# Optimization experiments

Hardware: AMD Instinct MI355X
Metric: run time of the kernel (lower is better)

Reference implementation:

```python
import jax, jax.numpy as jnp
import numpy as np

B, N, D, H, L = 2, 1024, 256, 4, 6
DH = D // H          # head dim 64
RDIM = DH // 2       # AxialRotaryEmbedding dim = 32 -> output feature size DH
THETA = 0.01


def setup_inputs() -> dict:
    key = jax.random.key(0)
    ks = iter(jax.random.split(key, 80))
    def nrm(shape, s=1.0):
        return jax.random.normal(next(ks), shape, jnp.float32) * s
    size = jnp.array([1024.0, 768.0], jnp.float32)
    inp = {
        'kpts0': jax.random.uniform(next(ks), (B, N, 2), jnp.float32) * size,
        'kpts1': jax.random.uniform(next(ks), (B, N, 2), jnp.float32) * size,
        'desc0': nrm((B, N, D)),
        'desc1': nrm((B, N, D)),
        'fx': 1.0 / (THETA ** (jnp.arange(0, RDIM, 2, dtype=jnp.float32) / RDIM)),
        'fy': 1.0 / (THETA ** (jnp.arange(0, RDIM, 2, dtype=jnp.float32) / RDIM)),
    }
    s = D ** -0.5
    for p in ('s', 'c'):
        inp[f'{p}_Wqk'] = nrm((L, D, D), s); inp[f'{p}_bqk'] = jnp.zeros((L, D))
        inp[f'{p}_Wv'] = nrm((L, D, D), s);  inp[f'{p}_bv'] = jnp.zeros((L, D))
        inp[f'{p}_Wo'] = nrm((L, D, D), s);  inp[f'{p}_bo'] = jnp.zeros((L, D))
        inp[f'{p}_W1'] = nrm((L, 2 * D, 2 * D), (2 * D) ** -0.5); inp[f'{p}_b1'] = jnp.zeros((L, 2 * D))
        inp[f'{p}_g'] = jnp.ones((L, 2 * D)); inp[f'{p}_be'] = jnp.zeros((L, 2 * D))
        inp[f'{p}_W2'] = nrm((L, 2 * D, D), (2 * D) ** -0.5); inp[f'{p}_b2'] = jnp.zeros((L, D))
    inp['Wp'] = nrm((D, D), s); inp['bp'] = jnp.zeros((D,))
    inp['Wm'] = nrm((D, 1), s); inp['bm'] = jnp.zeros((1,))
    return inp


def reference(kpts0, kpts1, desc0, desc1, fx, fy,
              s_Wqk, s_bqk, s_Wv, s_bv, s_Wo, s_bo, s_W1, s_b1, s_g, s_be, s_W2, s_b2,
              c_Wqk, c_bqk, c_Wv, c_bv, c_Wo, c_bo, c_W1, c_b1, c_g, c_be, c_W2, c_b2,
              Wp, bp, Wm, bm):
    size = jnp.array([1024.0, 768.0], jnp.float32)
    norm_k = lambda k: (k - size / 2) / (size.max() / 2)
    heads = lambda t: t.reshape(t.shape[0], t.shape[1], H, DH)

    def rope(pos):  # pos [B,N,2] -> cos,sin [B,N,1,DH]
        f = jnp.concatenate([jnp.repeat(pos[..., 0:1] * fx, 2, -1),
                             jnp.repeat(pos[..., 1:2] * fy, 2, -1)], -1)[:, :, None, :]
        return jnp.cos(f), jnp.sin(f)

    def rot_half(x):  # pairs (x0,x1) -> (-x1,x0)
        return jnp.stack([-x[..., 1::2], x[..., 0::2]], -1).reshape(x.shape)

    def ln(x, g, b):
        mu = x.mean(-1, keepdims=True)
        v = ((x - mu) ** 2).mean(-1, keepdims=True)
        return (x - mu) / jnp.sqrt(v + 1e-5) * g + b

    def ffn(x, m, W1, b1, g, be, W2, b2):  # x + MLP(LN(concat(x,m)))
        h = jnp.concatenate([x, m], -1) @ W1 + b1
        return x + jax.nn.gelu(ln(h, g, be), approximate=False) @ W2 + b2

    cs0, sn0 = rope(norm_k(kpts0))
    cs1, sn1 = rope(norm_k(kpts1))
    x0, x1 = desc0, desc1
    for i in range(L):
        def self_blk(x, cs, sn):  # rotary self-attention, shared qk projection
            qk = heads(x @ s_Wqk[i] + s_bqk[i])
            qr = qk * cs + rot_half(qk) * sn
            v = heads(x @ s_Wv[i] + s_bv[i])
            a = jax.nn.softmax(jnp.einsum('bnhd,bmhd->bhnm', qr, qr) * DH ** -0.5, -1)
            m = jnp.einsum('bhnm,bmhd->bnhd', a, v).reshape(x.shape) @ s_Wo[i] + s_bo[i]
            return ffn(x, m, s_W1[i], s_b1[i], s_g[i], s_be[i], s_W2[i], s_b2[i])
        x0 = self_blk(x0, cs0, sn0)
        x1 = self_blk(x1, cs1, sn1)
        # bidirectional cross-attention (CrossTransformer math path)
        sc = (DH ** -0.5) ** 0.5
        qk0 = heads(x0 @ c_Wqk[i] + c_bqk[i]) * sc
        qk1 = heads(x1 @ c_Wqk[i] + c_bqk[i]) * sc
        v0 = heads(x0 @ c_Wv[i] + c_bv[i])
        v1 = heads(x1 @ c_Wv[i] + c_bv[i])
        sim = jnp.einsum('bnhd,bmhd->bhnm', qk0, qk1)
        m0 = jnp.einsum('bhnm,bmhd->bnhd', jax.nn.softmax(sim, -1), v1).reshape(x0.shape) @ c_Wo[i] + c_bo[i]
        m1 = jnp.einsum('bhnm,bnhd->bmhd', jax.nn.softmax(sim, 2), v0).reshape(x1.shape) @ c_Wo[i] + c_bo[i]
        x0 = ffn(x0, m0, c_W1[i], c_b1[i], c_g[i], c_be[i], c_W2[i], c_b2[i])
        x1 = ffn(x1, m1, c_W1[i], c_b1[i], c_g[i], c_be[i], c_W2[i], c_b2[i])
    # MatchAssignment: sigmoid log double softmax (temp=None, use_sqrt=False -> r=1)
    md0 = (x0 @ Wp + bp) / D ** 0.25
    md1 = (x1 @ Wp + bp) / D ** 0.25
    sim = jnp.einsum('bmd,bnd->bmn', md0, md1)
    z0 = x0 @ Wm + bm  # [B,N,1]
    z1 = x1 @ Wm + bm
    cert = jax.nn.log_sigmoid(z0) + jnp.swapaxes(jax.nn.log_sigmoid(z1), 1, 2)
    core = jax.nn.log_softmax(sim, -1) + jax.nn.log_softmax(sim, 1) + cert
    scores = jnp.zeros((sim.shape[0], N + 1, N + 1), sim.dtype)
    scores = scores.at[:, :N, :N].set(core)
    scores = scores.at[:, :N, N].set(jax.nn.log_sigmoid(-z0[..., 0]))
    scores = scores.at[:, N, :N].set(jax.nn.log_sigmoid(-z1[..., 0]))
    return scores
```

## Files before the change

kernel.cpp:

```cpp
#include <hip/hip_runtime.h>
#include <hip/hip_bf16.h>
#include <math.h>

#define NB 2
#define NN 1024
#define ND 256
#define NL 6
#define NP (NN + 1)

typedef unsigned short u16;
typedef __attribute__((ext_vector_type(8))) short bf16x8;
typedef __attribute__((ext_vector_type(4))) float f32x4;

__device__ __forceinline__ u16 f2b(float f) {
    union { float f; unsigned u; } v; v.f = f;
    unsigned r = v.u + 0x7FFFu + ((v.u >> 16) & 1u);
    return (u16)(r >> 16);
}
__device__ __forceinline__ float b2f(u16 b) {
    union { unsigned u; float f; } v; v.u = ((unsigned)b) << 16;
    return v.f;
}
__device__ __forceinline__ float logsigf(float x) {
    return (x >= 0.f) ? -log1pf(expf(-x)) : (x - log1pf(expf(x)));
}

__global__ void rope_cs_kernel(const float* __restrict__ k0p, const float* __restrict__ k1p,
                               const float* __restrict__ fx, const float* __restrict__ fy,
                               float* __restrict__ cs, float* __restrict__ sn) {
    int idx = blockIdx.x * 256 + threadIdx.x;
    int row = idx >> 6, j = idx & 63;
    const float* kp = (row < 2048) ? k0p + (size_t)row * 2 : k1p + (size_t)(row - 2048) * 2;
    float kx = kp[0], ky = kp[1];
    float f;
    if (j < 32) f = ((kx - 512.f) * (1.f / 512.f)) * fx[j >> 1];
    else        f = ((ky - 384.f) * (1.f / 512.f)) * fy[(j - 32) >> 1];
    cs[idx] = cosf(f);
    sn[idx] = sinf(f);
}

__global__ void copyconv_kernel(const float* __restrict__ d0, const float* __restrict__ d1,
                                float* __restrict__ outf, u16* __restrict__ outb) {
    int i = blockIdx.x * 256 + threadIdx.x;
    float v = (i < 524288) ? d0[i] : d1[i - 524288];
    outf[i] = v; outb[i] = f2b(v);
}

struct WP6 {
    const float* s[6];
    u16* d[6];
    unsigned long long oz[6];
};
__global__ void wconvM_kernel(WP6 w, int perT, int K, int N) {
    __shared__ float t[32][33];
    int z = blockIdx.z;
    int p = z / perT, l = z - p * perT;
    const float* W = w.s[p] + (size_t)l * K * N;
    u16* Wt = w.d[p] + (size_t)l * w.oz[p];
    int k0 = blockIdx.y * 32, n0 = blockIdx.x * 32;
    int tx = threadIdx.x, ty = threadIdx.y;
    for (int i = 0; i < 32; i += 8)
        t[ty + i][tx] = W[(size_t)(k0 + ty + i) * N + n0 + tx];
    __syncthreads();
    for (int i = 0; i < 32; i += 8)
        Wt[(size_t)(n0 + ty + i) * K + k0 + tx] = f2b(t[tx][ty + i]);
}

__global__ void biaspack2_kernel(const float* __restrict__ sbqk, const float* __restrict__ sbv,
                                 const float* __restrict__ cbqk, const float* __restrict__ cbv,
                                 float* __restrict__ out) {
    int idx = blockIdx.x * 256 + threadIdx.x;
    if (idx >= 12 * 512) return;
    int z = idx >> 9, c = idx & 511;
    const float* q = (z < 6) ? sbqk + z * 256 : cbqk + (z - 6) * 256;
    const float* v = (z < 6) ? sbv + z * 256 : cbv + (z - 6) * 256;
    out[idx] = (c < 256) ? q[c] : v[c - 256];
}

__global__ __launch_bounds__(256)
void wfuse_kernel(const float* __restrict__ sWo, const float* __restrict__ sW1,
                  const float* __restrict__ cWo, const float* __restrict__ cW1,
                  u16* __restrict__ wfs, u16* __restrict__ wfc) {
    __shared__ u16 As[64 * 72];
    __shared__ u16 Bs[64 * 72];
    int z = blockIdx.z;
    const float* Wo = (z < 6) ? sWo + (size_t)z * 65536 : cWo + (size_t)(z - 6) * 65536;
    const float* W1 = (z < 6) ? sW1 + (size_t)z * 262144 : cW1 + (size_t)(z - 6) * 262144;
    u16* out = (z < 6) ? wfs + (size_t)z * 262144 : wfc + (size_t)(z - 6) * 262144;
    int n0 = blockIdx.y * 64, a0 = blockIdx.x * 64;
    int tid = threadIdx.x, lane = tid & 63, wave = tid >> 6;
    int wm = (wave >> 1) * 32, wn = (wave & 1) * 32;
    int l15 = lane & 15, l4 = lane >> 4;
    f32x4 acc[2][2] = {};
    for (int j0 = 0; j0 < 256; j0 += 64) {
        {
            int nl = tid & 63, jg = tid >> 6;
#pragma unroll
            for (int q = 0; q < 16; ++q) {
                int j = jg * 16 + q;
                As[nl * 72 + j] = f2b(W1[(size_t)(256 + j0 + j) * 512 + n0 + nl]);
            }
        }
        {
            int jl = tid & 63, ag = tid >> 6;
#pragma unroll
            for (int q = 0; q < 16; ++q) {
                int a = ag * 16 + q;
                Bs[a * 72 + jl] = f2b(Wo[(size_t)(a0 + a) * 256 + j0 + jl]);
            }
        }
        __syncthreads();
#pragma unroll
        for (int ks = 0; ks < 2; ++ks) {
            bf16x8 af0 = *(bf16x8*)&As[(wm + l15) * 72 + ks * 32 + l4 * 8];
            bf16x8 af1 = *(bf16x8*)&As[(wm + 16 + l15) * 72 + ks * 32 + l4 * 8];
            bf16x8 bf0 = *(bf16x8*)&Bs[(wn + l15) * 72 + ks * 32 + l4 * 8];
            bf16x8 bf1 = *(bf16x8*)&Bs[(wn + 16 + l15) * 72 + ks * 32 + l4 * 8];
            acc[0][0] = __builtin_amdgcn_mfma_f32_16x16x32_bf16(af0, bf0, acc[0][0], 0, 0, 0);
            acc[0][1] = __builtin_amdgcn_mfma_f32_16x16x32_bf16(af0, bf1, acc[0][1], 0, 0, 0);
            acc[1][0] = __builtin_amdgcn_mfma_f32_16x16x32_bf16(af1, bf0, acc[1][0], 0, 0, 0);
            acc[1][1] = __builtin_amdgcn_mfma_f32_16x16x32_bf16(af1, bf1, acc[1][1], 0, 0, 0);
        }
        __syncthreads();
    }
#pragma unroll
    for (int mi = 0; mi < 2; ++mi)
#pragma unroll
        for (int ni = 0; ni < 2; ++ni)
#pragma unroll
            for (int j = 0; j < 4; ++j) {
                int r = n0 + wm + mi * 16 + l4 * 4 + j;
                int c = a0 + wn + ni * 16 + l15;
                out[(size_t)r * 512 + 256 + c] = f2b(acc[mi][ni][j]);
            }
}

__global__ void bfuse_kernel(const float* __restrict__ sb1, const float* __restrict__ sbo,
                             const float* __restrict__ sW1, const float* __restrict__ cb1,
                             const float* __restrict__ cbo, const float* __restrict__ cW1,
                             float* __restrict__ bfb) {
    int z = blockIdx.y;
    int n = blockIdx.x * 256 + threadIdx.x;
    const float* b1 = (z < 6) ? sb1 + z * 512 : cb1 + (z - 6) * 512;
    const float* bo = (z < 6) ? sbo + z * 256 : cbo + (z - 6) * 256;
    const float* W1 = (z < 6) ? sW1 + (size_t)z * 262144 : cW1 + (size_t)(z - 6) * 262144;
    float acc = b1[n];
    for (int a = 0; a < 256; ++a) acc += bo[a] * W1[(size_t)(256 + a) * 512 + n];
    bfb[z * 512 + n] = acc;
}

__global__ __launch_bounds__(256)
void gemm_mfma(const u16* __restrict__ A, const u16* __restrict__ Bt,
               const float* __restrict__ bias, const float* __restrict__ res,
               float* __restrict__ Cf, u16* __restrict__ Cb,
               int M, int N, int K, float scale_lo, float scale_hi,
               const float* __restrict__ csp, const float* __restrict__ snp) {
    __shared__ u16 As[2][64 * 72];
    __shared__ u16 Bs[2][64 * 72];
    int tid = threadIdx.x;
    int lane = tid & 63, wave = tid >> 6;
    int row0 = blockIdx.y * 64, col0 = blockIdx.x * 64;
    int wm = (wave >> 1) * 32, wn = (wave & 1) * 32;
    int l15 = lane & 15, l4 = lane >> 4;
    f32x4 acc[2][2] = {};
    int srl = tid >> 3, sc8 = (tid & 7) * 8;

    auto loadA = [&](int k0, int it) -> bf16x8 {
        return *(const bf16x8*)&A[(size_t)(row0 + srl + it * 32) * K + k0 + sc8];
    };
    auto loadB = [&](int k0, int it) -> bf16x8 {
        return *(const bf16x8*)&Bt[(size_t)(col0 + srl + it * 32) * K + k0 + sc8];
    };

    bf16x8 rA0 = loadA(0, 0), rA1 = loadA(0, 1);
    bf16x8 rB0 = loadB(0, 0), rB1 = loadB(0, 1);
    *(bf16x8*)&As[0][srl * 72 + sc8] = rA0;
    *(bf16x8*)&As[0][(srl + 32) * 72 + sc8] = rA1;
    *(bf16x8*)&Bs[0][srl * 72 + sc8] = rB0;
    *(bf16x8*)&Bs[0][(srl + 32) * 72 + sc8] = rB1;
    __syncthreads();

    int nt = K >> 6;
    for (int t = 0; t < nt; ++t) {
        int buf = t & 1;
        bool more = (t + 1) < nt;
        if (more) {
            rA0 = loadA((t + 1) * 64, 0); rA1 = loadA((t + 1) * 64, 1);
            rB0 = loadB((t + 1) * 64, 0); rB1 = loadB((t + 1) * 64, 1);
        }
#pragma unroll
        for (int ks = 0; ks < 2; ++ks) {
            bf16x8 a0 = *(bf16x8*)&As[buf][(wm + l15) * 72 + ks * 32 + l4 * 8];
            bf16x8 a1 = *(bf16x8*)&As[buf][(wm + 16 + l15) * 72 + ks * 32 + l4 * 8];
            bf16x8 b0 = *(bf16x8*)&Bs[buf][(wn + l15) * 72 + ks * 32 + l4 * 8];
            bf16x8 b1 = *(bf16x8*)&Bs[buf][(wn + 16 + l15) * 72 + ks * 32 + l4 * 8];
            acc[0][0] = __builtin_amdgcn_mfma_f32_16x16x32_bf16(a0, b0, acc[0][0], 0, 0, 0);
            acc[0][1] = __builtin_amdgcn_mfma_f32_16x16x32_bf16(a0, b1, acc[0][1], 0, 0, 0);
            acc[1][0] = __builtin_amdgcn_mfma_f32_16x16x32_bf16(a1, b0, acc[1][0], 0, 0, 0);
            acc[1][1] = __builtin_amdgcn_mfma_f32_16x16x32_bf16(a1, b1, acc[1][1], 0, 0, 0);
        }
        if (more) {
            int nb = buf ^ 1;
            *(bf16x8*)&As[nb][srl * 72 + sc8] = rA0;
            *(bf16x8*)&As[nb][(srl + 32) * 72 + sc8] = rA1;
            *(bf16x8*)&Bs[nb][srl * 72 + sc8] = rB0;
            *(bf16x8*)&Bs[nb][(srl + 32) * 72 + sc8] = rB1;
        }
        __syncthreads();
    }
#pragma unroll
    for (int mi = 0; mi < 2; ++mi)
#pragma unroll
        for (int ni = 0; ni < 2; ++ni)
#pragma unroll
            for (int j = 0; j < 4; ++j) {
                int r = row0 + wm + mi * 16 + l4 * 4 + j;
                int c = col0 + wn + ni * 16 + l15;
                float v = acc[mi][ni][j] + (bias ? bias[c] : 0.f);
                float pn = __shfl_xor(v, 1);
                if (csp && c < 256) {
                    float cc = csp[(size_t)r * 64 + (c & 63)];
                    float ss = snp[(size_t)r * 64 + (c & 63)];
                    v = (c & 1) ? (v * cc + pn * ss) : (v * cc - pn * ss);
                }
                v *= (c < 256) ? scale_lo : scale_hi;
                if (res) v += res[(size_t)r * N + c];
                if (Cf) Cf[(size_t)r * N + c] = v;
                if (Cb) Cb[(size_t)r * N + c] = f2b(v);
            }
}

__global__ __launch_bounds__(256)
void gemm_w1f(const u16* __restrict__ xb, const float* __restrict__ Op,
              const float* __restrict__ mp, const float* __restrict__ lp,
              const u16* __restrict__ Bt, const float* __restrict__ bias,
              u16* __restrict__ hb) {
    __shared__ u16 As[2][64 * 72];
    __shared__ u16 Bs[2][64 * 72];
    const int N = 512, K = 512;
    int tid = threadIdx.x;
    int lane = tid & 63, wave = tid >> 6;
    int row0 = blockIdx.y * 64, col0 = blockIdx.x * 64;
    int wm = (wave >> 1) * 32, wn = (wave & 1) * 32;
    int l15 = lane & 15, l4 = lane >> 4;
    f32x4 acc[2][2] = {};
    int srl = tid >> 3, sc8 = (tid & 7) * 8;

    auto loadA = [&](int k0, int it) -> bf16x8 {
        int rg = row0 + srl + it * 32;
        int kg = k0 + sc8;
        if (kg < 256) return *(const bf16x8*)&xb[(size_t)rg * 256 + kg];
        int kg2 = kg - 256;
        int h = kg2 >> 6, d0 = kg2 & 63;
        int t = rg >> 11, bb = (rg >> 10) & 1, iq = rg & 1023;
        int ri = (t * 8 + bb * 4 + h) * 1024 + iq;
        size_t base0 = (size_t)ri * 64 + d0;
        size_t base1 = base0 + (size_t)16384 * 64;
        f32x4 a0 = *(const f32x4*)&Op[base0];
        f32x4 a1 = *(const f32x4*)&Op[base0 + 4];
        f32x4 c0 = *(const f32x4*)&Op[base1];
        f32x4 c1 = *(const f32x4*)&Op[base1 + 4];
        float m0 = mp[ri], m1 = mp[16384 + ri];
        float l0 = lp[ri], l1 = lp[16384 + ri];
        float mf = fmaxf(m0, m1);
        float e0 = __expf(m0 - mf), e1 = __expf(m1 - mf);
        float inv = 1.f / (l0 * e0 + l1 * e1);
        e0 *= inv; e1 *= inv;
        u16 o[8];
#pragma unroll
        for (int e = 0; e < 4; ++e) {
            o[e] = f2b(a0[e] * e0 + c0[e] * e1);
            o[4 + e] = f2b(a1[e] * e0 + c1[e] * e1);
        }
        return *(bf16x8*)o;
    };
    auto loadB = [&](int k0, int it) -> bf16x8 {
        return *(const bf16x8*)&Bt[(size_t)(col0 + srl + it * 32) * K + k0 + sc8];
    };

    bf16x8 rA0 = loadA(0, 0), rA1 = loadA(0, 1);
    bf16x8 rB0 = loadB(0, 0), rB1 = loadB(0, 1);
    *(bf16x8*)&As[0][srl * 72 + sc8] = rA0;
    *(bf16x8*)&As[0][(srl + 32) * 72 + sc8] = rA1;
    *(bf16x8*)&Bs[0][srl * 72 + sc8] = rB0;
    *(bf16x8*)&Bs[0][(srl + 32) * 72 + sc8] = rB1;
    __syncthreads();

    for (int t = 0; t < 8; ++t) {
        int buf = t & 1;
        bool more = (t + 1) < 8;
        if (more) {
            rA0 = loadA((t + 1) * 64, 0); rA1 = loadA((t + 1) * 64, 1);
            rB0 = loadB((t + 1) * 64, 0); rB1 = loadB((t + 1) * 64, 1);
        }
#pragma unroll
        for (int ks = 0; ks < 2; ++ks) {
            bf16x8 a0 = *(bf16x8*)&As[buf][(wm + l15) * 72 + ks * 32 + l4 * 8];
            bf16x8 a1 = *(bf16x8*)&As[buf][(wm + 16 + l15) * 72 + ks * 32 + l4 * 8];
            bf16x8 b0 = *(bf16x8*)&Bs[buf][(wn + l15) * 72 + ks * 32 + l4 * 8];
            bf16x8 b1 = *(bf16x8*)&Bs[buf][(wn + 16 + l15) * 72 + ks * 32 + l4 * 8];
            acc[0][0] = __builtin_amdgcn_mfma_f32_16x16x32_bf16(a0, b0, acc[0][0], 0, 0, 0);
            acc[0][1] = __builtin_amdgcn_mfma_f32_16x16x32_bf16(a0, b1, acc[0][1], 0, 0, 0);
            acc[1][0] = __builtin_amdgcn_mfma_f32_16x16x32_bf16(a1, b0, acc[1][0], 0, 0, 0);
            acc[1][1] = __builtin_amdgcn_mfma_f32_16x16x32_bf16(a1, b1, acc[1][1], 0, 0, 0);
        }
        if (more) {
            int nb = buf ^ 1;
            *(bf16x8*)&As[nb][srl * 72 + sc8] = rA0;
            *(bf16x8*)&As[nb][(srl + 32) * 72 + sc8] = rA1;
            *(bf16x8*)&Bs[nb][srl * 72 + sc8] = rB0;
            *(bf16x8*)&Bs[nb][(srl + 32) * 72 + sc8] = rB1;
        }
        __syncthreads();
    }
#pragma unroll
    for (int mi = 0; mi < 2; ++mi)
#pragma unroll
        for (int ni = 0; ni < 2; ++ni)
#pragma unroll
            for (int j = 0; j < 4; ++j) {
                int r = row0 + wm + mi * 16 + l4 * 4 + j;
                int c = col0 + wn + ni * 16 + l15;
                hb[(size_t)r * N + c] = f2b(acc[mi][ni][j] + bias[c]);
            }
}

__global__ __launch_bounds__(256)
void ln_gelu_wave(const u16* __restrict__ hb, const float* __restrict__ g,
                  const float* __restrict__ be, u16* __restrict__ out) {
    int wave = threadIdx.x >> 6, lane = threadIdx.x & 63;
    int row = blockIdx.x * 4 + wave;
    const u16* p = hb + (size_t)row * 512 + lane * 8;
    bf16x8 v = *(const bf16x8*)p;
    float f[8];
    float sum = 0.f, ss = 0.f;
#pragma unroll
    for (int e = 0; e < 8; ++e) {
        f[e] = b2f(((u16*)&v)[e]);
        sum += f[e]; ss += f[e] * f[e];
    }
#pragma unroll
    for (int d = 1; d < 64; d <<= 1) {
        sum += __shfl_xor(sum, d);
        ss  += __shfl_xor(ss, d);
    }
    float mu = sum * (1.f / 512.f);
    float rstd = rsqrtf(ss * (1.f / 512.f) - mu * mu + 1e-5f);
    f32x4 g0 = *(const f32x4*)&g[lane * 8];
    f32x4 g1 = *(const f32x4*)&g[lane * 8 + 4];
    f32x4 b0 = *(const f32x4*)&be[lane * 8];
    f32x4 b1 = *(const f32x4*)&be[lane * 8 + 4];
    u16 o[8];
#pragma unroll
    for (int e = 0; e < 8; ++e) {
        float gg = (e < 4) ? g0[e] : g1[e - 4];
        float bb = (e < 4) ? b0[e] : b1[e - 4];
        float y = (f[e] - mu) * rstd * gg + bb;
        o[e] = f2b(0.5f * y * (1.f + erff(y * 0.70710678118654752f)));
    }
    *(bf16x8*)(out + (size_t)row * 512 + lane * 8) = *(bf16x8*)o;
}

#define QSTR 72
#define VDSTR 1032
#define VBUFE (4 * VDSTR)

__global__ __launch_bounds__(256)
void flash_kernel(const u16* __restrict__ Qp, const u16* __restrict__ Vp,
                  float* __restrict__ Op, float* __restrict__ mp, float* __restrict__ lp,
                  int kswap) {
    __shared__ u16 Qs[64 * QSTR];
    __shared__ u16 Ks[2][64 * QSTR];
    __shared__ u16 Vs[2][VBUFE];
    __shared__ u16 Ps[64 * QSTR];
    int y = blockIdx.z;
    int half = blockIdx.y;
    int t = y >> 3, b = (y >> 2) & 1, h = y & 3;
    int qR = t * 2048 + b * 1024;
    int kt = kswap ? (1 - t) : t;
    int kR = kt * 2048 + b * 1024 + half * 512;
    int i0 = blockIdx.x * 64;
    int tid = threadIdx.x, lane = tid & 63, wave = tid >> 6;
    int l15 = lane & 15, l4 = lane >> 4;
    int wm = wave * 16;
    int srl = tid >> 3, sc8 = (tid & 7) * 8;

    const u16* Qbase = Qp + (size_t)(qR + i0) * 512 + h * 64;
    const u16* Kbase = Qp + (size_t)kR * 512 + h * 64;
    const u16* Vbase = Vp + (size_t)kR * 512 + h * 64;

#pragma unroll
    for (int it = 0; it < 2; ++it) {
        int rr = srl + it * 32;
        *(bf16x8*)&Qs[rr * QSTR + sc8] = *(const bf16x8*)&Qbase[(size_t)rr * 512 + sc8];
        *(bf16x8*)&Ks[0][rr * QSTR + sc8] = *(const bf16x8*)&Kbase[(size_t)rr * 512 + sc8];
        bf16x8 v = *(const bf16x8*)&Vbase[(size_t)rr * 512 + sc8];
        *(bf16x8*)&Vs[0][(sc8 >> 4) * VDSTR + rr * 16 + (sc8 & 15)] = v;
    }
    __syncthreads();

    bf16x8 qf[2];
    qf[0] = *(bf16x8*)&Qs[(wm + l15) * QSTR + l4 * 8];
    qf[1] = *(bf16x8*)&Qs[(wm + l15) * QSTR + 32 + l4 * 8];

    float m[4], l[4];
    f32x4 accO[4] = {};
#pragma unroll
    for (int j = 0; j < 4; ++j) { m[j] = -1e30f; l[j] = 0.f; }

    for (int j0 = 0; j0 < 512; j0 += 64) {
        int buf = (j0 >> 6) & 1;
        bool more = (j0 + 64) < 512;
        bf16x8 nK0, nK1, nV0, nV1;
        if (more) {
            nK0 = *(const bf16x8*)&Kbase[(size_t)(j0 + 64 + srl) * 512 + sc8];
            nK1 = *(const bf16x8*)&Kbase[(size_t)(j0 + 96 + srl) * 512 + sc8];
            nV0 = *(const bf16x8*)&Vbase[(size_t)(j0 + 64 + srl) * 512 + sc8];
            nV1 = *(const bf16x8*)&Vbase[(size_t)(j0 + 96 + srl) * 512 + sc8];
        }
        f32x4 accS[4] = {};
#pragma unroll
        for (int ks = 0; ks < 2; ++ks) {
#pragma unroll
            for (int n = 0; n < 4; ++n) {
                bf16x8 bb = *(bf16x8*)&Ks[buf][(n * 16 + l15) * QSTR + ks * 32 + l4 * 8];
                accS[n] = __builtin_amdgcn_mfma_f32_16x16x32_bf16(qf[ks], bb, accS[n], 0, 0, 0);
            }
        }
        float p[4][4];
#pragma unroll
        for (int j = 0; j < 4; ++j) {
            float tm = fmaxf(fmaxf(accS[0][j], accS[1][j]), fmaxf(accS[2][j], accS[3][j]));
#pragma unroll
            for (int d = 1; d < 16; d <<= 1) tm = fmaxf(tm, __shfl_xor(tm, d));
            float mnew = fmaxf(m[j], tm);
            float rr = __expf(m[j] - mnew);
            float ts = 0.f;
#pragma unroll
            for (int n = 0; n < 4; ++n) {
                float pv = __expf(accS[n][j] - mnew);
                p[n][j] = pv; ts += pv;
            }
#pragma unroll
            for (int d = 1; d < 16; d <<= 1) ts += __shfl_xor(ts, d);
            l[j] = l[j] * rr + ts;
            m[j] = mnew;
#pragma unroll
            for (int n = 0; n < 4; ++n) accO[n][j] *= rr;
        }
#pragma unroll
        for (int n = 0; n < 4; ++n) {
            int kv = n * 16 + l15;
            int c = (kv & 32) + (((kv >> 2) & 3) << 3) + (((kv >> 4) & 1) << 2) + (kv & 3);
#pragma unroll
            for (int j = 0; j < 4; ++j)
                Ps[(wm + l4 * 4 + j) * QSTR + c] = f2b(p[n][j]);
        }
#pragma unroll
        for (int ks = 0; ks < 2; ++ks) {
            bf16x8 a = *(bf16x8*)&Ps[(wm + l15) * QSTR + ks * 32 + l4 * 8];
#pragma unroll
            for (int n = 0; n < 4; ++n) {
                unsigned va = (unsigned)(size_t)(&Vs[buf][n * VDSTR]) + ks * 1024 + lane * 8;
                unsigned long long q0, q1;
                asm volatile("ds_read_b64_tr_b16 %0, %2\n\t"
                             "ds_read_b64_tr_b16 %1, %2 offset:512\n\t"
                             "s_waitcnt lgkmcnt(0)"
                             : "=&v"(q0), "=&v"(q1) : "v"(va) : "memory");
                union { unsigned long long q[2]; bf16x8 v; } uu;
                uu.q[0] = q0; uu.q[1] = q1;
                accO[n] = __builtin_amdgcn_mfma_f32_16x16x32_bf16(a, uu.v, accO[n], 0, 0, 0);
            }
        }
        if (more) {
            int nb = buf ^ 1;
            *(bf16x8*)&Ks[nb][srl * QSTR + sc8] = nK0;
            *(bf16x8*)&Ks[nb][(srl + 32) * QSTR + sc8] = nK1;
            *(bf16x8*)&Vs[nb][(sc8 >> 4) * VDSTR + srl * 16 + (sc8 & 15)] = nV0;
            *(bf16x8*)&Vs[nb][(sc8 >> 4) * VDSTR + (srl + 32) * 16 + (sc8 & 15)] = nV1;
        }
        __syncthreads();
    }
    size_t obase = (size_t)(half * 16 + y) * 1024 + i0;
#pragma unroll
    for (int n = 0; n < 4; ++n)
#pragma unroll
        for (int j = 0; j < 4; ++j) {
            int r = wm + l4 * 4 + j;
            Op[(obase + r) * 64 + n * 16 + l15] = accO[n][j];
        }
    if (l15 == 0) {
#pragma unroll
        for (int j = 0; j < 4; ++j) {
            int r = wm + l4 * 4 + j;
            mp[obase + r] = m[j];
            lp[obase + r] = l[j];
        }
    }
}

__global__ void rowstats_kernel(const float* __restrict__ S, float* __restrict__ rm,
                                float* __restrict__ rs, int ncols) {
    __shared__ float sb[256];
    int row = blockIdx.x, tid = threadIdx.x;
    const float* p = S + (size_t)row * ncols;
    float m = -1e30f;
    for (int j = tid; j < ncols; j += 256) m = fmaxf(m, p[j]);
    sb[tid] = m; __syncthreads();
    for (int s = 128; s > 0; s >>= 1) { if (tid < s) sb[tid] = fmaxf(sb[tid], sb[tid + s]); __syncthreads(); }
    m = sb[0]; __syncthreads();
    float s = 0;
    for (int j = tid; j < ncols; j += 256) s += __expf(p[j] - m);
    sb[tid] = s; __syncthreads();
    for (int st = 128; st > 0; st >>= 1) { if (tid < st) sb[tid] += sb[tid + st]; __syncthreads(); }
    if (tid == 0) { rm[row] = m; rs[row] = sb[0]; }
}

#define CSCH 8
__global__ void colstats_part(const float* __restrict__ S, float* __restrict__ pm,
                              float* __restrict__ ps) {
    int mat = blockIdx.z;
    int j = blockIdx.x * 256 + threadIdx.x;
    int r0 = blockIdx.y * (NN / CSCH);
    const float* p = S + (size_t)mat * NN * NN + (size_t)r0 * NN + j;
    float m = -1e30f;
    for (int i = 0; i < NN / CSCH; ++i) m = fmaxf(m, p[(size_t)i * NN]);
    float s = 0;
    for (int i = 0; i < NN / CSCH; ++i) s += __expf(p[(size_t)i * NN] - m);
    int o = (mat * CSCH + blockIdx.y) * NN + j;
    pm[o] = m; ps[o] = s;
}
__global__ void colstats_red(const float* __restrict__ pm, const float* __restrict__ ps,
                             float* __restrict__ cm, float* __restrict__ cs) {
    int idx = blockIdx.x * 256 + threadIdx.x;
    int mat = idx >> 10, j = idx & 1023;
    float m = -1e30f;
#pragma unroll
    for (int k = 0; k < CSCH; ++k) m = fmaxf(m, pm[(mat * CSCH + k) * NN + j]);
    float s = 0;
#pragma unroll
    for (int k = 0; k < CSCH; ++k)
        s += ps[(mat * CSCH + k) * NN + j] * __expf(pm[(mat * CSCH + k) * NN + j] - m);
    cm[idx] = m; cs[idx] = s;
}

__global__ void zproj_kernel(const float* __restrict__ X, const float* __restrict__ Wm,
                             const float* __restrict__ bm, float* __restrict__ z) {
    __shared__ float sb[256];
    int row = blockIdx.x, tid = threadIdx.x;
    float v = X[(size_t)row * 256 + tid] * Wm[tid];
    sb[tid] = v; __syncthreads();
    for (int s = 128; s > 0; s >>= 1) { if (tid < s) sb[tid] += sb[tid + s]; __syncthreads(); }
    if (tid == 0) z[row] = sb[0] + bm[0];
}

__global__ void assemble_kernel(const float* __restrict__ sim2, const float* __restrict__ z0,
                                const float* __restrict__ z1, const float* __restrict__ rm,
                                const float* __restrict__ rs, const float* __restrict__ cm,
                                const float* __restrict__ cs, float* __restrict__ out) {
    int idx = blockIdx.x * 256 + threadIdx.x;
    if (idx >= NB * NP * NP) return;
    int b = idx / (NP * NP);
    int rem = idx - b * NP * NP;
    int i = rem / NP, j = rem - i * NP;
    float v;
    if (i < NN && j < NN) {
        float s = sim2[((size_t)b * NN + i) * NN + j];
        float lr = s - rm[b * NN + i] - logf(rs[b * NN + i]);
        float lc = s - cm[b * NN + j] - logf(cs[b * NN + j]);
        v = lr + lc + logsigf(z0[b * NN + i]) + logsigf(z1[b * NN + j]);
    } else if (i < NN) {
        v = logsigf(-z0[b * NN + i]);
    } else if (j < NN) {
        v = logsigf(-z1[b * NN + j]);
    } else {
        v = 0.f;
    }
    out[idx] = v;
}

extern "C" void kernel_launch(void* const* d_in, const int* in_sizes, int n_in,
                              void* d_out, int out_size, void* d_ws, size_t ws_size,
                              hipStream_t stream) {
    auto in = [&](int i) { return (const float*)d_in[i]; };
    const float* kpts0 = in(0);
    const float* kpts1 = in(1);
    const float* desc0 = in(2);
    const float* desc1 = in(3);
    const float* fx = in(4);
    const float* fy = in(5);
    const float* sWqk = in(6);  const float* sbqk = in(7);
    const float* sWv  = in(8);  const float* sbv  = in(9);
    const float* sWo  = in(10); const float* sbo  = in(11);
    const float* sW1  = in(12); const float* sb1  = in(13);
    const float* sg   = in(14); const float* sbe  = in(15);
    const float* sW2  = in(16); const float* sb2  = in(17);
    const float* cWqk = in(18); const float* cbqk = in(19);
    const float* cWv  = in(20); const float* cbv  = in(21);
    const float* cWo  = in(22); const float* cbo  = in(23);
    const float* cW1  = in(24); const float* cb1  = in(25);
    const float* cg   = in(26); const float* cbe  = in(27);
    const float* cW2  = in(28); const float* cb2  = in(29);
    const float* Wp = in(30); const float* bp = in(31);
    const float* Wm = in(32); const float* bm = in(33);

    const int Mst = 2 * NB * NN;
    const size_t SND = (size_t)Mst * ND;

    char* base = (char*)d_ws;
    size_t off = 0;
    auto allocf = [&](size_t n) { float* p = (float*)(base + off); off += ((n * 4 + 255) & ~(size_t)255); return p; };
    auto allocb = [&](size_t n) { u16* p = (u16*)(base + off);   off += ((n * 2 + 255) & ~(size_t)255); return p; };

    float* x    = allocf(SND);
    float* cst  = allocf((size_t)Mst * 64);
    float* snt  = allocf((size_t)Mst * 64);
    float* simb = allocf((size_t)NB * NN * NN);
    float* Opb  = allocf((size_t)2 * 16384 * 64);
    float* mpb  = allocf((size_t)2 * 16384);
    float* lpb  = allocf((size_t)2 * 16384);
    float* z    = allocf(Mst);
    float* st0  = allocf(2048);
    float* st1  = allocf(2048);
    float* st2  = allocf(2048);
    float* st3  = allocf(2048);
    float* pmb  = allocf((size_t)NB * CSCH * NN);
    float* psb  = allocf((size_t)NB * CSCH * NN);
    float* bqv  = allocf((size_t)12 * 512);
    float* bfb  = allocf((size_t)12 * 512);

    u16* xb    = allocb(SND);
    u16* tQVb  = allocb((size_t)Mst * 512);
    u16* attnb = allocb(SND);
    u16* hb    = allocb((size_t)Mst * 512);
    u16* hgb   = allocb((size_t)Mst * 512);
    u16* wsqv = allocb((size_t)NL * 512 * 256);
    u16* wcqv = allocb((size_t)NL * 512 * 256);
    u16* wfs  = allocb((size_t)NL * 512 * 512);
    u16* wfc  = allocb((size_t)NL * 512 * 512);
    u16* wsw2 = allocb((size_t)NL * 512 * 256);
    u16* wcw2 = allocb((size_t)NL * 512 * 256);
    u16* wpb  = allocb((size_t)256 * 256);

    {
        WP6 wa = {};
        wa.s[0] = sWqk; wa.d[0] = wsqv;             wa.oz[0] = 512 * 256;
        wa.s[1] = sWv;  wa.d[1] = wsqv + 256 * 256; wa.oz[1] = 512 * 256;
        wa.s[2] = cWqk; wa.d[2] = wcqv;             wa.oz[2] = 512 * 256;
        wa.s[3] = cWv;  wa.d[3] = wcqv + 256 * 256; wa.oz[3] = 512 * 256;
        wa.s[4] = Wp;   wa.d[4] = wpb;              wa.oz[4] = 256 * 256;
        wconvM_kernel<<<dim3(8, 8, 25), dim3(32, 8), 0, stream>>>(wa, 6, 256, 256);
        WP6 wb = {};
        wb.s[0] = sW1; wb.d[0] = wfs; wb.oz[0] = 512 * 512;
        wb.s[1] = cW1; wb.d[1] = wfc; wb.oz[1] = 512 * 512;
        wconvM_kernel<<<dim3(16, 8, 12), dim3(32, 8), 0, stream>>>(wb, 6, 512, 512);
        WP6 wc = {};
        wc.s[0] = sW2; wc.d[0] = wsw2; wc.oz[0] = 512 * 256;
        wc.s[1] = cW2; wc.d[1] = wcw2; wc.oz[1] = 512 * 256;
        wconvM_kernel<<<dim3(8, 16, 12), dim3(32, 8), 0, stream>>>(wc, 6, 512, 256);
    }
    wfuse_kernel<<<dim3(4, 8, 12), 256, 0, stream>>>(sWo, sW1, cWo, cW1, wfs, wfc);
    bfuse_kernel<<<dim3(2, 12), 256, 0, stream>>>(sb1, sbo, sW1, cb1, cbo, cW1, bfb);
    biaspack2_kernel<<<(12 * 512 + 255) / 256, 256, 0, stream>>>(sbqk, sbv, cbqk, cbv, bqv);

    rope_cs_kernel<<<1024, 256, 0, stream>>>(kpts0, kpts1, fx, fy, cst, snt);
    copyconv_kernel<<<4096, 256, 0, stream>>>(desc0, desc1, x, xb);

    auto gemm = [&](const u16* A, const u16* Bt, const float* bias, const float* res,
                    float* Cf, u16* Cb, int M, int N, int K,
                    float slo, float shi, const float* csp, const float* snp) {
        gemm_mfma<<<dim3(N / 64, M / 64), 256, 0, stream>>>(A, Bt, bias, res, Cf, Cb,
                                                            M, N, K, slo, shi, csp, snp);
    };

    const float sc = 0.35355339059327379f;

    for (int i = 0; i < NL; ++i) {
        const size_t oQV = (size_t)i * 512 * 256;
        const size_t oWF = (size_t)i * 512 * 512;
        const size_t oW2 = (size_t)i * 512 * 256;

        gemm(xb, wsqv + oQV, bqv + i * 512, nullptr, nullptr, tQVb,
             Mst, 512, 256, sc, 1.f, cst, snt);
        flash_kernel<<<dim3(16, 2, 16), 256, 0, stream>>>(tQVb, tQVb + 256, Opb, mpb, lpb, 0);
        gemm_w1f<<<dim3(8, 64), 256, 0, stream>>>(xb, Opb, mpb, lpb, wfs + oWF, bfb + i * 512, hb);
        ln_gelu_wave<<<Mst / 4, 256, 0, stream>>>(hb, sg + i * 512, sbe + i * 512, hgb);
        gemm(hgb, wsw2 + oW2, sb2 + i * ND, x, x, xb,
             Mst, 256, 512, 1.f, 1.f, nullptr, nullptr);

        gemm(xb, wcqv + oQV, bqv + (6 + i) * 512, nullptr, nullptr, tQVb,
             Mst, 512, 256, sc, 1.f, nullptr, nullptr);
        flash_kernel<<<dim3(16, 2, 16), 256, 0, stream>>>(tQVb, tQVb + 256, Opb, mpb, lpb, 1);
        gemm_w1f<<<dim3(8, 64), 256, 0, stream>>>(xb, Opb, mpb, lpb, wfc + oWF, bfb + (6 + i) * 512, hb);
        ln_gelu_wave<<<Mst / 4, 256, 0, stream>>>(hb, cg + i * 512, cbe + i * 512, hgb);
        gemm(hgb, wcw2 + oW2, cb2 + i * ND, x, x, xb,
             Mst, 256, 512, 1.f, 1.f, nullptr, nullptr);
    }

    gemm(xb, wpb, bp, nullptr, nullptr, attnb,
         Mst, 256, 256, 0.25f, 0.25f, nullptr, nullptr);
    zproj_kernel<<<Mst, 256, 0, stream>>>(x, Wm, bm, z);
    for (int b = 0; b < NB; ++b) {
        gemm(attnb + (size_t)b * 1024 * 256,
             attnb + (size_t)(2048 + b * 1024) * 256, nullptr, nullptr,
             simb + (size_t)b * NN * NN, nullptr,
             1024, 1024, 256, 1.f, 1.f, nullptr, nullptr);
    }
    rowstats_kernel<<<NB * NN, 256, 0, stream>>>(simb, st0, st1, NN);
    colstats_part<<<dim3(NN / 256, CSCH, NB), 256, 0, stream>>>(simb, pmb, psb);
    colstats_red<<<(NB * NN) / 256, 256, 0, stream>>>(pmb, psb, st2, st3);
    int total = NB * NP * NP;
    assemble_kernel<<<(total + 255) / 256, 256, 0, stream>>>(simb, z, z + 2048, st0, st1,
                                                             st2, st3, (float*)d_out);
}
```

Before: 1.045 ms.

## Split flash attention keys four ways with separate combine kernel

Flash attention now splits each query tile's keys into four chunks instead of two, which doubles the number of blocks, and loads Q fragments straight from global memory into registers. A new combine kernel merges the four partial softmax results into a bf16 buffer, and the generic GEMM reads its K dimension from two source pointers in place of the specialised fused W1 GEMM. The two per-batch similarity GEMMs are merged into one launch using a z-dimension batch. The aim is better occupancy in attention, at the cost of an extra kernel launch and an intermediate write and read per attention stage.

After: 1.048 ms. No clear change (+0.3%).

```diff
diff --git a/kernel.cpp b/kernel.cpp
--- a/kernel.cpp
+++ b/kernel.cpp
@@ -7,6 +7,7 @@
 #define ND 256
 #define NL 6
 #define NP (NN + 1)
+#define NSP 4
 
 typedef unsigned short u16;
 typedef __attribute__((ext_vector_type(8))) short bf16x8;
@@ -150,13 +151,17 @@
 }
 
 __global__ __launch_bounds__(256)
-void gemm_mfma(const u16* __restrict__ A, const u16* __restrict__ Bt,
-               const float* __restrict__ bias, const float* __restrict__ res,
-               float* __restrict__ Cf, u16* __restrict__ Cb,
+void gemm_mfma(const u16* __restrict__ A, const u16* __restrict__ A2,
+               const u16* __restrict__ Bt, const float* __restrict__ bias,
+               const float* __restrict__ res, float* __restrict__ Cf, u16* __restrict__ Cb,
                int M, int N, int K, float scale_lo, float scale_hi,
-               const float* __restrict__ csp, const float* __restrict__ snp) {
+               const float* __restrict__ csp, const float* __restrict__ snp,
+               long zsA, long zsB, long zsC) {
     __shared__ u16 As[2][64 * 72];
     __shared__ u16 Bs[2][64 * 72];
+    int zb = blockIdx.z;
+    A += (size_t)zb * zsA;
+    Bt += (size_t)zb * zsB;
     int tid = threadIdx.x;
     int lane = tid & 63, wave = tid >> 6;
     int row0 = blockIdx.y * 64, col0 = blockIdx.x * 64;
@@ -166,7 +171,12 @@
     int srl = tid >> 3, sc8 = (tid & 7) * 8;
 
     auto loadA = [&](int k0, int it) -> bf16x8 {
-        return *(const bf16x8*)&A[(size_t)(row0 + srl + it * 32) * K + k0 + sc8];
+        int rr = row0 + srl + it * 32;
+        int kg = k0 + sc8;
+        const u16* src;
+        if (A2) src = (kg < 256) ? &A[(size_t)rr * 256 + kg] : &A2[(size_t)rr * 256 + kg - 256];
+        else    src = &A[(size_t)rr * K + kg];
+        return *(const bf16x8*)src;
     };
     auto loadB = [&](int k0, int it) -> bf16x8 {
         return *(const bf16x8*)&Bt[(size_t)(col0 + srl + it * 32) * K + k0 + sc8];
@@ -225,104 +235,45 @@
                 }
                 v *= (c < 256) ? scale_lo : scale_hi;
                 if (res) v += res[(size_t)r * N + c];
-                if (Cf) Cf[(size_t)r * N + c] = v;
+                if (Cf) Cf[(size_t)zb * zsC + (size_t)r * N + c] = v;
                 if (Cb) Cb[(size_t)r * N + c] = f2b(v);
             }
 }
 
 __global__ __launch_bounds__(256)
-void gemm_w1f(const u16* __restrict__ xb, const float* __restrict__ Op,
-              const float* __restrict__ mp, const float* __restrict__ lp,
-              const u16* __restrict__ Bt, const float* __restrict__ bias,
-              u16* __restrict__ hb) {
-    __shared__ u16 As[2][64 * 72];
-    __shared__ u16 Bs[2][64 * 72];
-    const int N = 512, K = 512;
-    int tid = threadIdx.x;
-    int lane = tid & 63, wave = tid >> 6;
-    int row0 = blockIdx.y * 64, col0 = blockIdx.x * 64;
-    int wm = (wave >> 1) * 32, wn = (wave & 1) * 32;
-    int l15 = lane & 15, l4 = lane >> 4;
-    f32x4 acc[2][2] = {};
-    int srl = tid >> 3, sc8 = (tid & 7) * 8;
-
-    auto loadA = [&](int k0, int it) -> bf16x8 {
-        int rg = row0 + srl + it * 32;
-        int kg = k0 + sc8;
-        if (kg < 256) return *(const bf16x8*)&xb[(size_t)rg * 256 + kg];
-        int kg2 = kg - 256;
-        int h = kg2 >> 6, d0 = kg2 & 63;
-        int t = rg >> 11, bb = (rg >> 10) & 1, iq = rg & 1023;
-        int ri = (t * 8 + bb * 4 + h) * 1024 + iq;
-        size_t base0 = (size_t)ri * 64 + d0;
-        size_t base1 = base0 + (size_t)16384 * 64;
-        f32x4 a0 = *(const f32x4*)&Op[base0];
-        f32x4 a1 = *(const f32x4*)&Op[base0 + 4];
-        f32x4 c0 = *(const f32x4*)&Op[base1];
-        f32x4 c1 = *(const f32x4*)&Op[base1 + 4];
-        float m0 = mp[ri], m1 = mp[16384 + ri];
-        float l0 = lp[ri], l1 = lp[16384 + ri];
-        float mf = fmaxf(m0, m1);
-        float e0 = __expf(m0 - mf), e1 = __expf(m1 - mf);
-        float inv = 1.f / (l0 * e0 + l1 * e1);
-        e0 *= inv; e1 *= inv;
-        u16 o[8];
-#pragma unroll
-        for (int e = 0; e < 4; ++e) {
-            o[e] = f2b(a0[e] * e0 + c0[e] * e1);
-            o[4 + e] = f2b(a1[e] * e0 + c1[e] * e1);
-        }
-        return *(bf16x8*)o;
-    };
-    auto loadB = [&](int k0, int it) -> bf16x8 {
-        return *(const bf16x8*)&Bt[(size_t)(col0 + srl + it * 32) * K + k0 + sc8];
-    };
-
-    bf16x8 rA0 = loadA(0, 0), rA1 = loadA(0, 1);
-    bf16x8 rB0 = loadB(0, 0), rB1 = loadB(0, 1);
-    *(bf16x8*)&As[0][srl * 72 + sc8] = rA0;
-    *(bf16x8*)&As[0][(srl + 32) * 72 + sc8] = rA1;
-    *(bf16x8*)&Bs[0][srl * 72 + sc8] = rB0;
-    *(bf16x8*)&Bs[0][(srl + 32) * 72 + sc8] = rB1;
-    __syncthreads();
-
-    for (int t = 0; t < 8; ++t) {
-        int buf = t & 1;
-        bool more = (t + 1) < 8;
-        if (more) {
-            rA0 = loadA((t + 1) * 64, 0); rA1 = loadA((t + 1) * 64, 1);
-            rB0 = loadB((t + 1) * 64, 0); rB1 = loadB((t + 1) * 64, 1);
-        }
-#pragma unroll
-        for (int ks = 0; ks < 2; ++ks) {
-            bf16x8 a0 = *(bf16x8*)&As[buf][(wm + l15) * 72 + ks * 32 + l4 * 8];
-            bf16x8 a1 = *(bf16x8*)&As[buf][(wm + 16 + l15) * 72 + ks * 32 + l4 * 8];
-            bf16x8 b0 = *(bf16x8*)&Bs[buf][(wn + l15) * 72 + ks * 32 + l4 * 8];
-            bf16x8 b1 = *(bf16x8*)&Bs[buf][(wn + 16 + l15) * 72 + ks * 32 + l4 * 8];
-            acc[0][0] = __builtin_amdgcn_mfma_f32_16x16x32_bf16(a0, b0, acc[0][0], 0, 0, 0);
-            acc[0][1] = __builtin_amdgcn_mfma_f32_16x16x32_bf16(a0, b1, acc[0][1], 0, 0, 0);
-            acc[1][0] = __builtin_amdgcn_mfma_f32_16x16x32_bf16(a1, b0, acc[1][0], 0, 0, 0);
-            acc[1][1] = __builtin_amdgcn_mfma_f32_16x16x32_bf16(a1, b1, acc[1][1], 0, 0, 0);
-        }
-        if (more) {
-            int nb = buf ^ 1;
-            *(bf16x8*)&As[nb][srl * 72 + sc8] = rA0;
-            *(bf16x8*)&As[nb][(srl + 32) * 72 + sc8] = rA1;
-            *(bf16x8*)&Bs[nb][srl * 72 + sc8] = rB0;
-            *(bf16x8*)&Bs[nb][(srl + 32) * 72 + sc8] = rB1;
-        }
-        __syncthreads();
-    }
-#pragma unroll
-    for (int mi = 0; mi < 2; ++mi)
-#pragma unroll
-        for (int ni = 0; ni < 2; ++ni)
-#pragma unroll
-            for (int j = 0; j < 4; ++j) {
-                int r = row0 + wm + mi * 16 + l4 * 4 + j;
-                int c = col0 + wn + ni * 16 + l15;
-                hb[(size_t)r * N + c] = f2b(acc[mi][ni][j] + bias[c]);
-            }
+void combine4_kernel(const float* __restrict__ Op, const float* __restrict__ mp,
+                     const float* __restrict__ lp, u16* __restrict__ Ocomb) {
+    int idx = blockIdx.x * 256 + threadIdx.x;
+    int ri = idx >> 3, dseg = idx & 7;
+    int y = ri >> 10, iq = ri & 1023;
+    int t = y >> 3, b = (y >> 2) & 1, h = y & 3;
+    int rg = t * 2048 + b * 1024 + iq;
+    float m[NSP], l[NSP];
+    float mf = -1e30f;
+#pragma unroll
+    for (int s = 0; s < NSP; ++s) {
+        m[s] = mp[s * 16384 + ri];
+        l[s] = lp[s * 16384 + ri];
+        mf = fmaxf(mf, m[s]);
+    }
+    float e[NSP], denom = 0.f;
+#pragma unroll
+    for (int s = 0; s < NSP; ++s) { e[s] = __expf(m[s] - mf); denom += l[s] * e[s]; }
+    float inv = 1.f / denom;
+    float o[8] = {};
+#pragma unroll
+    for (int s = 0; s < NSP; ++s) {
+        size_t base = ((size_t)(s * 16384 + ri)) * 64 + dseg * 8;
+        f32x4 a0 = *(const f32x4*)&Op[base];
+        f32x4 a1 = *(const f32x4*)&Op[base + 4];
+        float w = e[s] * inv;
+#pragma unroll
+        for (int q = 0; q < 4; ++q) { o[q] += a0[q] * w; o[4 + q] += a1[q] * w; }
+    }
+    u16 ob[8];
+#pragma unroll
+    for (int q = 0; q < 8; ++q) ob[q] = f2b(o[q]);
+    *(bf16x8*)&Ocomb[(size_t)rg * 256 + h * 64 + dseg * 8] = *(bf16x8*)ob;
 }
 
 __global__ __launch_bounds__(256)
@@ -369,7 +320,6 @@
 void flash_kernel(const u16* __restrict__ Qp, const u16* __restrict__ Vp,
                   float* __restrict__ Op, float* __restrict__ mp, float* __restrict__ lp,
                   int kswap) {
-    __shared__ u16 Qs[64 * QSTR];
     __shared__ u16 Ks[2][64 * QSTR];
     __shared__ u16 Vs[2][VBUFE];
     __shared__ u16 Ps[64 * QSTR];
@@ -378,39 +328,39 @@
     int t = y >> 3, b = (y >> 2) & 1, h = y & 3;
     int qR = t * 2048 + b * 1024;
     int kt = kswap ? (1 - t) : t;
-    int kR = kt * 2048 + b * 1024 + half * 512;
+    int kR = kt * 2048 + b * 1024 + half * (NN / NSP);
     int i0 = blockIdx.x * 64;
     int tid = threadIdx.x, lane = tid & 63, wave = tid >> 6;
     int l15 = lane & 15, l4 = lane >> 4;
     int wm = wave * 16;
     int srl = tid >> 3, sc8 = (tid & 7) * 8;
 
-    const u16* Qbase = Qp + (size_t)(qR + i0) * 512 + h * 64;
     const u16* Kbase = Qp + (size_t)kR * 512 + h * 64;
     const u16* Vbase = Vp + (size_t)kR * 512 + h * 64;
 
 #pragma unroll
     for (int it = 0; it < 2; ++it) {
         int rr = srl + it * 32;
-        *(bf16x8*)&Qs[rr * QSTR + sc8] = *(const bf16x8*)&Qbase[(size_t)rr * 512 + sc8];
         *(bf16x8*)&Ks[0][rr * QSTR + sc8] = *(const bf16x8*)&Kbase[(size_t)rr * 512 + sc8];
         bf16x8 v = *(const bf16x8*)&Vbase[(size_t)rr * 512 + sc8];
         *(bf16x8*)&Vs[0][(sc8 >> 4) * VDSTR + rr * 16 + (sc8 & 15)] = v;
     }
+    bf16x8 qf[2];
+    {
+        const u16* qrow = Qp + (size_t)(qR + i0 + wm + l15) * 512 + h * 64;
+        qf[0] = *(const bf16x8*)&qrow[l4 * 8];
+        qf[1] = *(const bf16x8*)&qrow[32 + l4 * 8];
+    }
     __syncthreads();
-
-    bf16x8 qf[2];
-    qf[0] = *(bf16x8*)&Qs[(wm + l15) * QSTR + l4 * 8];
-    qf[1] = *(bf16x8*)&Qs[(wm + l15) * QSTR + 32 + l4 * 8];
 
     float m[4], l[4];
     f32x4 accO[4] = {};
 #pragma unroll
     for (int j = 0; j < 4; ++j) { m[j] = -1e30f; l[j] = 0.f; }
 
-    for (int j0 = 0; j0 < 512; j0 += 64) {
+    for (int j0 = 0; j0 < NN / NSP; j0 += 64) {
         int buf = (j0 >> 6) & 1;
-        bool more = (j0 + 64) < 512;
+        bool more = (j0 + 64) < NN / NSP;
         bf16x8 nK0, nK1, nV0, nV1;
         if (more) {
             nK0 = *(const bf16x8*)&Kbase[(size_t)(j0 + 64 + srl) * 512 + sc8];
@@ -616,9 +566,9 @@
     float* cst  = allocf((size_t)Mst * 64);
     float* snt  = allocf((size_t)Mst * 64);
     float* simb = allocf((size_t)NB * NN * NN);
-    float* Opb  = allocf((size_t)2 * 16384 * 64);
-    float* mpb  = allocf((size_t)2 * 16384);
-    float* lpb  = allocf((size_t)2 * 16384);
+    float* Opb  = allocf((size_t)NSP * 16384 * 64);
+    float* mpb  = allocf((size_t)NSP * 16384);
+    float* lpb  = allocf((size_t)NSP * 16384);
     float* z    = allocf(Mst);
     float* st0  = allocf(2048);
     float* st1  = allocf(2048);
@@ -631,6 +581,7 @@
 
     u16* xb    = allocb(SND);
     u16* tQVb  = allocb((size_t)Mst * 512);
+    u16* ocb   = allocb(SND);
     u16* attnb = allocb(SND);
     u16* hb    = allocb((size_t)Mst * 512);
     u16* hgb   = allocb((size_t)Mst * 512);
@@ -661,16 +612,17 @@
     }
     wfuse_kernel<<<dim3(4, 8, 12), 256, 0, stream>>>(sWo, sW1, cWo, cW1, wfs, wfc);
     bfuse_kernel<<<dim3(2, 12), 256, 0, stream>>>(sb1, sbo, sW1, cb1, cbo, cW1, bfb);
-    biaspack2_kernel<<<(12 * 512 + 255) / 256, 256, 0, stream>>>(sbqk, sbv, cbqk, cbv, bqv);
+    biaspack2_kernel<<<24, 256, 0, stream>>>(sbqk, sbv, cbqk, cbv, bqv);
 
     rope_cs_kernel<<<1024, 256, 0, stream>>>(kpts0, kpts1, fx, fy, cst, snt);
     copyconv_kernel<<<4096, 256, 0, stream>>>(desc0, desc1, x, xb);
 
-    auto gemm = [&](const u16* A, const u16* Bt, const float* bias, const float* res,
-                    float* Cf, u16* Cb, int M, int N, int K,
-                    float slo, float shi, const float* csp, const float* snp) {
-        gemm_mfma<<<dim3(N / 64, M / 64), 256, 0, stream>>>(A, Bt, bias, res, Cf, Cb,
-                                                            M, N, K, slo, shi, csp, snp);
+    auto gemm = [&](const u16* A, const u16* A2, const u16* Bt, const float* bias,
+                    const float* res, float* Cf, u16* Cb, int M, int N, int K,
+                    float slo, float shi, const float* csp, const float* snp,
+                    int nz = 1, long zsA = 0, long zsB = 0, long zsC = 0) {
+        gemm_mfma<<<dim3(N / 64, M / 64, nz), 256, 0, stream>>>(
+            A, A2, Bt, bias, res, Cf, Cb, M, N, K, slo, shi, csp, snp, zsA, zsB, zsC);
     };
 
     const float sc = 0.35355339059327379f;
@@ -680,32 +632,33 @@
         const size_t oWF = (size_t)i * 512 * 512;
         const size_t oW2 = (size_t)i * 512 * 256;
 
-        gemm(xb, wsqv + oQV, bqv + i * 512, nullptr, nullptr, tQVb,
+        gemm(xb, nullptr, wsqv + oQV, bqv + i * 512, nullptr, nullptr, tQVb,
              Mst, 512, 256, sc, 1.f, cst, snt);
-        flash_kernel<<<dim3(16, 2, 16), 256, 0, stream>>>(tQVb, tQVb + 256, Opb, mpb, lpb, 0);
-        gemm_w1f<<<dim3(8, 64), 256, 0, stream>>>(xb, Opb, mpb, lpb, wfs + oWF, bfb + i * 512, hb);
+        flash_kernel<<<dim3(16, NSP, 16), 256, 0, stream>>>(tQVb, tQVb + 256, Opb, mpb, lpb, 0);
+        combine4_kernel<<<512, 256, 0, stream>>>(Opb, mpb, lpb, ocb);
+        gemm(xb, ocb, wfs + oWF, bfb + i * 512, nullptr, nullptr, hb,
+             Mst, 512, 512, 1.f, 1.f, nullptr, nullptr);
         ln_gelu_wave<<<Mst / 4, 256, 0, stream>>>(hb, sg + i * 512, sbe + i * 512, hgb);
-        gemm(hgb, wsw2 + oW2, sb2 + i * ND, x, x, xb,
+        gemm(hgb, nullptr, wsw2 + oW2, sb2 + i * ND, x, x, xb,
              Mst, 256, 512, 1.f, 1.f, nullptr, nullptr);
 
-        gemm(xb, wcqv + oQV, bqv + (6 + i) * 512, nullptr, nullptr, tQVb,
+        gemm(xb, nullptr, wcqv + oQV, bqv + (6 + i) * 512, nullptr, nullptr, tQVb,
              Mst, 512, 256, sc, 1.f, nullptr, nullptr);
-        flash_kernel<<<dim3(16, 2, 16), 256, 0, stream>>>(tQVb, tQVb + 256, Opb, mpb, lpb, 1);
-        gemm_w1f<<<dim3(8, 64), 256, 0, stream>>>(xb, Opb, mpb, lpb, wfc + oWF, bfb + (6 + i) * 512, hb);
+        flash_kernel<<<dim3(16, NSP, 16), 256, 0, stream>>>(tQVb, tQVb + 256, Opb, mpb, lpb, 1);
+        combine4_kernel<<<512, 256, 0, stream>>>(Opb, mpb, lpb, ocb);
+        gemm(xb, ocb, wfc + oWF, bfb + (6 + i) * 512, nullptr, nullptr, hb,
+             Mst, 512, 512, 1.f, 1.f, nullptr, nullptr);
         ln_gelu_wave<<<Mst / 4, 256, 0, stream>>>(hb, cg + i * 512, cbe + i * 512, hgb);
-        gemm(hgb, wcw2 + oW2, cb2 + i * ND, x, x, xb,
+        gemm(hgb, nullptr, wcw2 + oW2, cb2 + i * ND, x, x, xb,
              Mst, 256, 512, 1.f, 1.f, nullptr, nullptr);
     }
 
-    gemm(xb, wpb, bp, nullptr, nullptr, attnb,
+    gemm(xb, nullptr, wpb, bp, nullptr, nullptr, attnb,
          Mst, 256, 256, 0.25f, 0.25f, nullptr, nullptr);
     zproj_kernel<<<Mst, 256, 0, stream>>>(x, Wm, bm, z);
-    for (int b = 0; b < NB; ++b) {
-        gemm(attnb + (size_t)b * 1024 * 256,
-             attnb + (size_t)(2048 + b * 1024) * 256, nullptr, nullptr,
-             simb + (size_t)b * NN * NN, nullptr,
-             1024, 1024, 256, 1.f, 1.f, nullptr, nullptr);
-    }
+    gemm(attnb, nullptr, attnb + (size_t)2048 * 256, nullptr, nullptr,
+         simb, nullptr, 1024, 1024, 256, 1.f, 1.f, nullptr, nullptr,
+         2, (long)1024 * 256, (long)1024 * 256, (long)NN * NN);
     rowstats_kernel<<<NB * NN, 256, 0, stream>>>(simb, st0, st1, NN);
     colstats_part<<<dim3(NN / 256, CSCH, NB), 256, 0, stream>>>(simb, pmb, psb);
     colstats_red<<<(NB * NN) / 256, 256, 0, stream>>>(pmb, psb, st2, st3);
```
